# Kernel tuning notes

Measured on AMD Instinct MI355X. Metric: run time of the kernel, lower is better.

## Reference

```python
import jax, jax.numpy as jnp
import numpy as np

B, N, DIM = 4, 16384, 256
H, D, G = 8, 64, 32  # heads, dim_head, slice_num; inner = H*D = 512


def setup_inputs() -> dict:
    key = jax.random.key(0)
    ks = jax.random.split(key, 12)
    inner = H * D
    s = lambda fan_in: 1.0 / np.sqrt(fan_in)
    inp = {
        "x": jax.random.normal(ks[0], (B, N, DIM), jnp.float32),
        # weights stored (in, out) so forward is x @ W + b
        "Wfx": jax.random.uniform(ks[1], (DIM, inner), jnp.float32, -s(DIM), s(DIM)),
        "bfx": jnp.zeros((inner,), jnp.float32),
        "Wx": jax.random.uniform(ks[2], (DIM, inner), jnp.float32, -s(DIM), s(DIM)),
        "bx": jnp.zeros((inner,), jnp.float32),
        "Wslice": jnp.linalg.qr(jax.random.normal(ks[3], (D, G), jnp.float32))[0],  # orthogonal init
        "bslice": jnp.zeros((G,), jnp.float32),
        "temperature": jnp.full((1, H, 1, 1), 0.5, jnp.float32),
        "Wq": jax.random.uniform(ks[4], (D, D), jnp.float32, -s(D), s(D)),
        "Wk": jax.random.uniform(ks[5], (D, D), jnp.float32, -s(D), s(D)),
        "Wv": jax.random.uniform(ks[6], (D, D), jnp.float32, -s(D), s(D)),
        "Wout": jax.random.uniform(ks[7], (inner, DIM), jnp.float32, -s(inner), s(inner)),
        "bout": jnp.zeros((DIM,), jnp.float32),
    }
    return inp


def reference(x, Wfx, bfx, Wx, bx, Wslice, bslice, temperature, Wq, Wk, Wv, Wout, bout):
    b, n, _ = x.shape
    # projections -> [B, H, N, D]
    fx_mid = (x @ Wfx + bfx).reshape(b, n, H, D).transpose(0, 2, 1, 3)
    x_mid = (x @ Wx + bx).reshape(b, n, H, D).transpose(0, 2, 1, 3)
    # soft slice assignment: [B, H, N, G]
    slice_logits = (x_mid @ Wslice + bslice) / temperature
    slice_weights = jax.nn.softmax(slice_logits, axis=-1)
    slice_norm = slice_weights.sum(axis=2)  # [B, H, G]
    # soft pooling to G slice tokens: [B, H, G, D]
    slice_token = jnp.einsum("bhnd,bhng->bhgd", fx_mid, slice_weights)
    slice_token = slice_token / (slice_norm[..., None] + 1e-5)
    # tiny attention over G tokens
    q = slice_token @ Wq
    k = slice_token @ Wk
    v = slice_token @ Wv
    scores = jnp.einsum("bhgd,bhkd->bhgk", q, k) / jnp.sqrt(jnp.asarray(D, q.dtype))
    attn = jax.nn.softmax(scores, axis=-1)
    out_slice = jnp.einsum("bhgk,bhkd->bhgd", attn, v)
    # scatter back to N points: [B, H, N, D] -> [B, N, H*D]
    out_x = jnp.einsum("bhgd,bhng->bhnd", out_slice, slice_weights)
    out_x = out_x.transpose(0, 2, 1, 3).reshape(b, n, H * D)
    return out_x @ Wout + bout
```

## Files before the change

kernel.cpp:

```cpp
#include <hip/hip_runtime.h>


typedef unsigned short u16;
typedef __attribute__((ext_vector_type(8))) unsigned short ushort8v;
typedef __attribute__((ext_vector_type(4))) unsigned short ushort4v;
typedef __attribute__((ext_vector_type(8))) short short8v;
typedef __attribute__((ext_vector_type(4))) float f32x4;

constexpr int Nc = 16384;
constexpr int BNc = 65536;

__device__ inline float b2f(u16 v) {
    union { unsigned int u; float f; } t; t.u = ((unsigned int)v) << 16; return t.f;
}
__device__ inline u16 f2b(float f) {
    union { float f; unsigned int u; } t; t.f = f;
    unsigned int u = t.u;
    return (u16)((u + 0x7fffu + ((u >> 16) & 1u)) >> 16);
}

__global__ __launch_bounds__(256) void k0_fold(
    const float* __restrict__ Wx, const float* __restrict__ Wslice,
    const float* __restrict__ bx, const float* __restrict__ bslice,
    u16* __restrict__ WxsT, float* __restrict__ bxs)
{
    int blk = blockIdx.x, tid = threadIdx.x;
    int h = tid >> 5, g = tid & 31;
    if (blk < 256) {
        int k = blk;
        float acc = 0.f;
        for (int d = 0; d < 64; d++)
            acc += Wx[k * 512 + h * 64 + d] * Wslice[d * 32 + g];
        WxsT[tid * 256 + k] = f2b(acc);
    } else {
        float acc = 0.f;
        for (int d = 0; d < 64; d++)
            acc += bx[h * 64 + d] * Wslice[d * 32 + g];
        bxs[tid] = acc + bslice[g];
    }
}

__global__ __launch_bounds__(256) void kprep_wfx(const float* __restrict__ Wfx,
                                                 u16* __restrict__ WfxT)
{
    int n = blockIdx.x, k = threadIdx.x;
    WfxT[n * 256 + k] = f2b(Wfx[k * 512 + n]);
}

__global__ __launch_bounds__(256) void kfrag(const u16* __restrict__ Ball,
                                             u16* __restrict__ Bf)
{
    int g = blockIdx.x * 256 + threadIdx.x;
    int pair = g >> 6, lane = g & 63;
    int t = pair >> 3, c = pair & 7;
    int n = t * 16 + (lane & 15);
    int k = c * 32 + (lane >> 4) * 8;
    ushort8v v = *(const ushort8v*)(Ball + (size_t)n * 256 + k);
    *(ushort8v*)(Bf + (size_t)((c * 48 + t) * 64 + lane) * 8) = v;
}

__global__ __launch_bounds__(512, 4) void kproj(
    const float* __restrict__ x, const u16* __restrict__ Bf,
    const float* __restrict__ bfx, const float* __restrict__ bxs,
    const float* __restrict__ temp,
    u16* __restrict__ fxT, u16* __restrict__ swb, u16* __restrict__ swT)
{
    __shared__ u16 As[32 * 256];
    int tid = threadIdx.x;
    int wave = tid >> 6, lane = tid & 63;
    int lm = lane & 15, quad = lane >> 4;
    int tg = blockIdx.y;
    int row0 = blockIdx.x * 32;
    int T0 = tg * 16 + 2 * wave;

    short8v breg0[8], breg1[8];
#pragma unroll
    for (int c = 0; c < 8; c++) {
        breg0[c] = *(const short8v*)(Bf + (size_t)((c * 48 + T0) * 64 + lane) * 8);
        breg1[c] = *(const short8v*)(Bf + (size_t)((c * 48 + T0 + 1) * 64 + lane) * 8);
    }

    {
        int row = tid >> 4, colg = tid & 15;
        const f32x4* src = (const f32x4*)(x + (size_t)(row0 + row) * 256 + colg * 16);
        f32x4 v0 = src[0], v1 = src[1], v2 = src[2], v3 = src[3];
        ushort8v o0, o1;
#pragma unroll
        for (int j = 0; j < 4; j++) {
            o0[j] = f2b(v0[j]); o0[4 + j] = f2b(v1[j]);
            o1[j] = f2b(v2[j]); o1[4 + j] = f2b(v3[j]);
        }
        int sw = (row & 7) << 4;
        char* base = (char*)As + row * 512;
        *(ushort8v*)(base + ((colg * 32) ^ sw)) = o0;
        *(ushort8v*)(base + ((colg * 32 + 16) ^ sw)) = o1;
    }
    __syncthreads();

    f32x4 acc00 = {}, acc01 = {}, acc10 = {}, acc11 = {};
    int swl = (lm & 7) << 4;
    const char* Arow0 = (const char*)As + lm * 512;
    const char* Arow1 = (const char*)As + (16 + lm) * 512;
#pragma unroll
    for (int c = 0; c < 8; c++) {
        int off = (c * 64 + quad * 16) ^ swl;
        short8v af0 = *(const short8v*)(Arow0 + off);
        short8v af1 = *(const short8v*)(Arow1 + off);
        acc00 = __builtin_amdgcn_mfma_f32_16x16x32_bf16(af0, breg0[c], acc00, 0, 0, 0);
        acc10 = __builtin_amdgcn_mfma_f32_16x16x32_bf16(af1, breg0[c], acc10, 0, 0, 0);
        acc01 = __builtin_amdgcn_mfma_f32_16x16x32_bf16(af0, breg1[c], acc01, 0, 0, 0);
        acc11 = __builtin_amdgcn_mfma_f32_16x16x32_bf16(af1, breg1[c], acc11, 0, 0, 0);
    }

    if (tg < 2) {
        int nbase = row0 + quad * 4;
#pragma unroll
        for (int i = 0; i < 2; i++) {
            int cc = (T0 + i) * 16 + lm;
            float bv = bfx[cc];
            const f32x4& a0 = i ? acc01 : acc00;
            const f32x4& a1 = i ? acc11 : acc10;
            ushort4v o0, o1;
#pragma unroll
            for (int r = 0; r < 4; r++) { o0[r] = f2b(a0[r] + bv); o1[r] = f2b(a1[r] + bv); }
            *(ushort4v*)(fxT + (size_t)cc * 65536 + nbase) = o0;
            *(ushort4v*)(fxT + (size_t)cc * 65536 + nbase + 16) = o1;
        }
    } else {
        int h = wave;
        int b = row0 >> 14;
        float it = 1.0f / temp[h];
        float bv0 = bxs[h * 32 + lm];
        float bv1 = bxs[h * 32 + 16 + lm];
        size_t gbase = (size_t)((b * 8 + h) * 32);
#pragma unroll
        for (int rf = 0; rf < 2; rf++) {
            const f32x4& A0 = rf ? acc10 : acc00;
            const f32x4& A1 = rf ? acc11 : acc01;
            int nlbase = (row0 & 16383) + rf * 16 + quad * 4;
            ushort4v p0, p1;
#pragma unroll
            for (int r = 0; r < 4; r++) {
                float v0 = (A0[r] + bv0) * it;
                float v1 = (A1[r] + bv1) * it;
                float m = fmaxf(v0, v1);
                m = fmaxf(m, __shfl_xor(m, 1));
                m = fmaxf(m, __shfl_xor(m, 2));
                m = fmaxf(m, __shfl_xor(m, 4));
                m = fmaxf(m, __shfl_xor(m, 8));
                float e0 = __expf(v0 - m), e1 = __expf(v1 - m);
                float s = e0 + e1;
                s += __shfl_xor(s, 1);
                s += __shfl_xor(s, 2);
                s += __shfl_xor(s, 4);
                s += __shfl_xor(s, 8);
                float rs = 1.0f / s;
                float w0 = e0 * rs, w1 = e1 * rs;
                int row = row0 + rf * 16 + quad * 4 + r;
                swb[(size_t)row * 256 + h * 32 + lm] = f2b(w0);
                swb[(size_t)row * 256 + h * 32 + 16 + lm] = f2b(w1);
                p0[r] = f2b(w0); p1[r] = f2b(w1);
            }
            *(ushort4v*)(swT + (gbase + lm) * 16384 + nlbase) = p0;
            *(ushort4v*)(swT + (gbase + 16 + lm) * 16384 + nlbase) = p1;
        }
    }
}

__global__ __launch_bounds__(256, 4) void kout(
    const u16* __restrict__ swb, const u16* __restrict__ ZTf,
    const float* __restrict__ bout, float* __restrict__ out)
{
    __shared__ u16 Bs[16 * 512];
    int tid = threadIdx.x;
    int wave = tid >> 6, lane = tid & 63;
    int lm = lane & 15, quad = lane >> 4;
    int row0 = blockIdx.x * 64;

    const u16* Abase = swb + (size_t)(row0 + wave * 16 + lm) * 256 + quad * 8;
    const u16* Zb    = ZTf + (size_t)(row0 >> 14) * 65536;

    f32x4 acc[16] = {};
    short8v af = *(const short8v*)(Abase);
    for (int c = 0; c < 8; c++) {
        const u16* src = Zb + (size_t)c * 8192 + (size_t)(wave * 4) * 512 + lane * 8;
#pragma unroll
        for (int i = 0; i < 4; i++) {
            ushort8v v = *(const ushort8v*)(src + i * 512);
            *(ushort8v*)&Bs[(wave * 4 + i) * 512 + lane * 8] = v;
        }
        short8v a_cur = af;
        if (c < 7) af = *(const short8v*)(Abase + c * 32 + 32);
        __syncthreads();
#pragma unroll
        for (int j = 0; j < 16; j++) {
            short8v bf = *(short8v*)&Bs[j * 512 + lane * 8];
            acc[j] = __builtin_amdgcn_mfma_f32_16x16x32_bf16(a_cur, bf, acc[j], 0, 0, 0);
        }
        __syncthreads();
    }
#pragma unroll
    for (int j = 0; j < 16; j++) {
        int cc = j * 16 + lm;
        float bv = bout[cc];
#pragma unroll
        for (int r = 0; r < 4; r++)
            out[(size_t)(row0 + wave * 16 + quad * 4 + r) * 256 + cc] = acc[j][r] + bv;
    }
}

__global__ __launch_bounds__(256, 4) void k4_token_mfma(
    const u16* __restrict__ swT, const u16* __restrict__ fxT,
    float* __restrict__ token_part, float* __restrict__ norm_part)
{
    __shared__ u16 As[32 * 256];
    __shared__ u16 Bs_[64 * 256];
    int bh = blockIdx.x, ky = blockIdx.y;
    int b = bh >> 3, h = bh & 7;
    int tid = threadIdx.x, wave = tid >> 6, lane = tid & 63;
    int lm = lane & 15, quad = lane >> 4;
    int mt = wave & 1, dp = wave >> 1;
    int lh = lane >> 5, lb = lane & 31;

#pragma unroll
    for (int i = 0; i < 4; i++) {
        int s = wave * 4 + i;
        int r = 2 * s + lh;
        int sw = ((lb * 16) ^ ((r & 7) << 4)) >> 1;
        const u16* src = swT + (size_t)(bh * 32 + r) * 16384 + ky * 256 + sw;
        __builtin_amdgcn_global_load_lds((const uint32_t*)src,
                                         (uint32_t*)(&As[s * 512]), 16, 0, 0);
    }
#pragma unroll
    for (int i = 0; i < 8; i++) {
        int s = wave * 8 + i;
        int r = 2 * s + lh;
        int sw = ((lb * 16) ^ ((r & 7) << 4)) >> 1;
        const u16* src = fxT + (size_t)(h * 64 + r) * 65536 + (size_t)b * 16384
                         + ky * 256 + sw;
        __builtin_amdgcn_global_load_lds((const uint32_t*)src,
                                         (uint32_t*)(&Bs_[s * 512]), 16, 0, 0);
    }
    __syncthreads();

    int rA = mt * 16 + lm;
    int rB0 = dp * 32 + lm, rB1 = rB0 + 16;
    const char* Ab  = (const char*)As  + rA  * 512;
    const char* Bb0 = (const char*)Bs_ + rB0 * 512;
    const char* Bb1 = (const char*)Bs_ + rB1 * 512;
    int swA  = (rA  & 7) << 4;
    int swB0 = (rB0 & 7) << 4;
    int swB1 = (rB1 & 7) << 4;

    f32x4 acc0 = {}, acc1 = {};
    float nacc = 0.f;
#pragma unroll
    for (int kk = 0; kk < 8; kk++) {
        int base = kk * 64 + quad * 16;
        short8v af = *(const short8v*)(Ab  + (base ^ swA));
        short8v b0 = *(const short8v*)(Bb0 + (base ^ swB0));
        short8v b1 = *(const short8v*)(Bb1 + (base ^ swB1));
        acc0 = __builtin_amdgcn_mfma_f32_16x16x32_bf16(af, b0, acc0, 0, 0, 0);
        acc1 = __builtin_amdgcn_mfma_f32_16x16x32_bf16(af, b1, acc1, 0, 0, 0);
        if (dp == 0) {
            ushort8v au = (ushort8v&)af;
#pragma unroll
            for (int j = 0; j < 8; j++) nacc += b2f(au[j]);
        }
    }
    float* tp = token_part + ((size_t)(ky * 32 + bh)) * 2048;
#pragma unroll
    for (int r = 0; r < 4; r++) {
        int g = mt * 16 + quad * 4 + r;
        tp[g * 64 + dp * 32 + lm] = acc0[r];
        tp[g * 64 + dp * 32 + 16 + lm] = acc1[r];
    }
    if (dp == 0) {
        nacc += __shfl_xor(nacc, 16);
        nacc += __shfl_xor(nacc, 32);
        if (lane < 16)
            norm_part[(ky * 32 + bh) * 32 + mt * 16 + lm] = nacc;
    }
}

__global__ __launch_bounds__(256) void k4b_reduce(
    const float* __restrict__ tp, const float* __restrict__ np,
    float* __restrict__ tl)
{
    int t = blockIdx.x * 256 + threadIdx.x;
    int bh = t >> 11, e = t & 2047, g = e >> 6;
    float ts = 0.f, ns = 0.f;
    for (int ch = 0; ch < 64; ch++) {
        ts += tp[((size_t)(ch * 32 + bh)) * 2048 + e];
        ns += np[(ch * 32 + bh) * 32 + g];
    }
    tl[t] = ts / (ns + 1e-5f);
}

__global__ __launch_bounds__(256) void k5_attn(
    const float* __restrict__ tlg,
    const float* __restrict__ Wq, const float* __restrict__ Wk, const float* __restrict__ Wv,
    float* __restrict__ out_slice)
{
    __shared__ float tl[32][64];
    __shared__ float ql[32][64], kl[32][64], vl[32][64];
    __shared__ float sl[32][33];
    int bh = blockIdx.x, tid = threadIdx.x;
    const float* tk = tlg + (size_t)bh * 2048;

#pragma unroll
    for (int j = 0; j < 8; j++) {
        int idx = j * 256 + tid;
        tl[idx >> 6][idx & 63] = tk[idx];
    }
    __syncthreads();
#pragma unroll
    for (int j = 0; j < 8; j++) {
        int idx = j * 256 + tid;
        int g = idx >> 6, d = idx & 63;
        float aq = 0.f, ak = 0.f, av = 0.f;
        for (int e = 0; e < 64; e++) {
            float t = tl[g][e];
            aq += t * Wq[e * 64 + d];
            ak += t * Wk[e * 64 + d];
            av += t * Wv[e * 64 + d];
        }
        ql[g][d] = aq; kl[g][d] = ak; vl[g][d] = av;
    }
    __syncthreads();
#pragma unroll
    for (int j = 0; j < 4; j++) {
        int idx = j * 256 + tid;
        int gq = idx >> 5, gk = idx & 31;
        float s = 0.f;
        for (int d = 0; d < 64; d++) s += ql[gq][d] * kl[gk][d];
        sl[gq][gk] = s * 0.125f;
    }
    __syncthreads();
    if (tid < 32) {
        float m = -1e30f;
        for (int k2 = 0; k2 < 32; k2++) m = fmaxf(m, sl[tid][k2]);
        float s = 0.f;
        for (int k2 = 0; k2 < 32; k2++) { float e = __expf(sl[tid][k2] - m); sl[tid][k2] = e; s += e; }
        float r = 1.0f / s;
        for (int k2 = 0; k2 < 32; k2++) sl[tid][k2] *= r;
    }
    __syncthreads();
#pragma unroll
    for (int j = 0; j < 8; j++) {
        int idx = j * 256 + tid;
        int g = idx >> 6, d = idx & 63;
        float a = 0.f;
        for (int k2 = 0; k2 < 32; k2++) a += sl[g][k2] * vl[k2][d];
        out_slice[(size_t)bh * 2048 + idx] = a;
    }
}

__global__ __launch_bounds__(256) void kZ(
    const float* __restrict__ os, const float* __restrict__ Wout,
    u16* __restrict__ ZTf)
{
    int b = blockIdx.x, cb = blockIdx.y;
    int t = threadIdx.x;
    int c = cb * 16 + (t & 15), kq = t >> 4;
    int tile = c >> 4, lm = c & 15;
    for (int k = kq * 16; k < kq * 16 + 16; k++) {
        int h = k >> 5, g = k & 31;
        const float* osr = os + ((size_t)(b * 8 + h)) * 2048 + g * 64;
        float acc = 0.f;
        for (int d = 0; d < 64; d++)
            acc += osr[d] * Wout[(h * 64 + d) * 256 + c];
        int ch = k >> 5, quad = (k >> 3) & 3, jj = k & 7;
        int lane = quad * 16 + lm;
        ZTf[((size_t)((b * 8 + ch) * 16 + tile)) * 512 + lane * 8 + jj] = f2b(acc);
    }
}

extern "C" void kernel_launch(void* const* d_in, const int* in_sizes, int n_in,
                              void* d_out, int out_size, void* d_ws, size_t ws_size,
                              hipStream_t stream)
{
    const float* x      = (const float*)d_in[0];
    const float* Wfx    = (const float*)d_in[1];
    const float* bfx    = (const float*)d_in[2];
    const float* Wx     = (const float*)d_in[3];
    const float* bx     = (const float*)d_in[4];
    const float* Wslice = (const float*)d_in[5];
    const float* bslice = (const float*)d_in[6];
    const float* temp   = (const float*)d_in[7];
    const float* Wq     = (const float*)d_in[8];
    const float* Wk     = (const float*)d_in[9];
    const float* Wv     = (const float*)d_in[10];
    const float* Wout   = (const float*)d_in[11];
    const float* bout   = (const float*)d_in[12];

    char* ws = (char*)d_ws;
    size_t off = 0;
    auto alloc = [&](size_t bytes) {
        void* p = ws + off;
        off = (off + bytes + 255) & ~(size_t)255;
        return p;
    };
    u16*   fxT   = (u16*)  alloc((size_t)512 * BNc * 2);
    u16*   swb   = (u16*)  alloc((size_t)BNc * 256 * 2);
    u16*   swT   = (u16*)  alloc((size_t)1024 * Nc * 2);
    float* tp    = (float*)alloc((size_t)2048 * 2048 * 4);
    float* np    = (float*)alloc((size_t)2048 * 32 * 4);
    float* tl    = (float*)alloc(65536 * 4);
    float* osl   = (float*)alloc(65536 * 4);
    u16*   ZTf   = (u16*)  alloc(4 * 65536 * 2);
    u16*   Ball  = (u16*)  alloc((size_t)768 * 256 * 2);
    u16*   Bfrg  = (u16*)  alloc((size_t)768 * 256 * 2);
    float* bxs   = (float*)alloc(256 * 4);

    u16* WfxT = Ball;
    u16* WxsT = Ball + (size_t)512 * 256;

    k0_fold<<<257, 256, 0, stream>>>(Wx, Wslice, bx, bslice, WxsT, bxs);
    kprep_wfx<<<512, 256, 0, stream>>>(Wfx, WfxT);
    kfrag<<<96, 256, 0, stream>>>(Ball, Bfrg);

    kproj<<<dim3(2048, 3), 512, 0, stream>>>(x, Bfrg, bfx, bxs, temp, fxT, swb, swT);

    k4_token_mfma<<<dim3(32, 64), 256, 0, stream>>>(swT, fxT, tp, np);
    k4b_reduce<<<256, 256, 0, stream>>>(tp, np, tl);
    k5_attn<<<32, 256, 0, stream>>>(tl, Wq, Wk, Wv, osl);
    kZ<<<dim3(4, 16), 256, 0, stream>>>(osl, Wout, ZTf);

    kout<<<1024, 256, 0, stream>>>(swb, ZTf, bout, (float*)d_out);
}
```

Baseline: 338.5 us.

## Restructure output GEMM to keep Z fragments in registers and stage swb tile in LDS

The final output kernel now uses 512-thread blocks over 32 rows. Each wave preloads its two 16-column slices of the per-batch Z matrix into registers. The 32x256 swb activation tile is staged once into swizzled LDS, which removes the per-chunk LDS staging of Z and the pair of barriers around every K step. A scheduling barrier is also added in the projection kernel so the weight register preloads are not interleaved with the x staging. The cost is higher register pressure and re-reading Z from global memory in every block.

```diff
diff --git a/kernel.cpp b/kernel.cpp
--- a/kernel.cpp
+++ b/kernel.cpp
@@ -79,6 +79,7 @@
         breg0[c] = *(const short8v*)(Bf + (size_t)((c * 48 + T0) * 64 + lane) * 8);
         breg1[c] = *(const short8v*)(Bf + (size_t)((c * 48 + T0 + 1) * 64 + lane) * 8);
     }
+    __builtin_amdgcn_sched_barrier(0);
 
     {
         int row = tid >> 4, colg = tid & 15;
@@ -167,45 +168,63 @@
     }
 }
 
-__global__ __launch_bounds__(256, 4) void kout(
+__global__ __launch_bounds__(512, 4) void kout(
     const u16* __restrict__ swb, const u16* __restrict__ ZTf,
     const float* __restrict__ bout, float* __restrict__ out)
 {
-    __shared__ u16 Bs[16 * 512];
+    __shared__ u16 As[32 * 256];
     int tid = threadIdx.x;
     int wave = tid >> 6, lane = tid & 63;
     int lm = lane & 15, quad = lane >> 4;
-    int row0 = blockIdx.x * 64;
-
-    const u16* Abase = swb + (size_t)(row0 + wave * 16 + lm) * 256 + quad * 8;
-    const u16* Zb    = ZTf + (size_t)(row0 >> 14) * 65536;
-
-    f32x4 acc[16] = {};
-    short8v af = *(const short8v*)(Abase);
+    int row0 = blockIdx.x * 32;
+    int T0 = 2 * wave;
+    int b = row0 >> 14;
+
+    const u16* Zb = ZTf + (size_t)b * 65536;
+    short8v breg0[8], breg1[8];
+#pragma unroll
     for (int c = 0; c < 8; c++) {
-        const u16* src = Zb + (size_t)c * 8192 + (size_t)(wave * 4) * 512 + lane * 8;
-#pragma unroll
-        for (int i = 0; i < 4; i++) {
-            ushort8v v = *(const ushort8v*)(src + i * 512);
-            *(ushort8v*)&Bs[(wave * 4 + i) * 512 + lane * 8] = v;
-        }
-        short8v a_cur = af;
-        if (c < 7) af = *(const short8v*)(Abase + c * 32 + 32);
-        __syncthreads();
-#pragma unroll
-        for (int j = 0; j < 16; j++) {
-            short8v bf = *(short8v*)&Bs[j * 512 + lane * 8];
-            acc[j] = __builtin_amdgcn_mfma_f32_16x16x32_bf16(a_cur, bf, acc[j], 0, 0, 0);
-        }
-        __syncthreads();
-    }
-#pragma unroll
-    for (int j = 0; j < 16; j++) {
-        int cc = j * 16 + lm;
-        float bv = bout[cc];
-#pragma unroll
-        for (int r = 0; r < 4; r++)
-            out[(size_t)(row0 + wave * 16 + quad * 4 + r) * 256 + cc] = acc[j][r] + bv;
+        breg0[c] = *(const short8v*)(Zb + (size_t)((c * 16 + T0) * 64 + lane) * 8);
+        breg1[c] = *(const short8v*)(Zb + (size_t)((c * 16 + T0 + 1) * 64 + lane) * 8);
+    }
+    __builtin_amdgcn_sched_barrier(0);
+
+    {
+        int row = tid >> 4, colg = tid & 15;
+        const ushort8v* src = (const ushort8v*)(swb + (size_t)(row0 + row) * 256 + colg * 16);
+        ushort8v v0 = src[0], v1 = src[1];
+        int sw = (row & 7) << 4;
+        char* base = (char*)As + row * 512;
+        *(ushort8v*)(base + ((colg * 32) ^ sw)) = v0;
+        *(ushort8v*)(base + ((colg * 32 + 16) ^ sw)) = v1;
+    }
+    __syncthreads();
+
+    f32x4 acc00 = {}, acc01 = {}, acc10 = {}, acc11 = {};
+    int swl = (lm & 7) << 4;
+    const char* Arow0 = (const char*)As + lm * 512;
+    const char* Arow1 = (const char*)As + (16 + lm) * 512;
+#pragma unroll
+    for (int c = 0; c < 8; c++) {
+        int off = (c * 64 + quad * 16) ^ swl;
+        short8v af0 = *(const short8v*)(Arow0 + off);
+        short8v af1 = *(const short8v*)(Arow1 + off);
+        acc00 = __builtin_amdgcn_mfma_f32_16x16x32_bf16(af0, breg0[c], acc00, 0, 0, 0);
+        acc10 = __builtin_amdgcn_mfma_f32_16x16x32_bf16(af1, breg0[c], acc10, 0, 0, 0);
+        acc01 = __builtin_amdgcn_mfma_f32_16x16x32_bf16(af0, breg1[c], acc01, 0, 0, 0);
+        acc11 = __builtin_amdgcn_mfma_f32_16x16x32_bf16(af1, breg1[c], acc11, 0, 0, 0);
+    }
+
+    int cc0 = T0 * 16 + lm, cc1 = cc0 + 16;
+    float bv0 = bout[cc0], bv1 = bout[cc1];
+#pragma unroll
+    for (int r = 0; r < 4; r++) {
+        int rowa = row0 + quad * 4 + r;
+        int rowb = rowa + 16;
+        out[(size_t)rowa * 256 + cc0] = acc00[r] + bv0;
+        out[(size_t)rowa * 256 + cc1] = acc01[r] + bv1;
+        out[(size_t)rowb * 256 + cc0] = acc10[r] + bv0;
+        out[(size_t)rowb * 256 + cc1] = acc11[r] + bv1;
     }
 }
 
@@ -427,5 +446,5 @@
     k5_attn<<<32, 256, 0, stream>>>(tl, Wq, Wk, Wv, osl);
     kZ<<<dim3(4, 16), 256, 0, stream>>>(osl, Wout, ZTf);
 
-    kout<<<1024, 256, 0, stream>>>(swb, ZTf, bout, (float*)d_out);
-}
+    kout<<<2048, 512, 0, stream>>>(swb, ZTf, bout, (float*)d_out);
+}
```

Measured after the change: 336.7 us. No clear change (-0.5%).
